# Kernel tuning notes

Measured on AMD Instinct MI355X. Metric: run time of the kernel, lower is better.

The kernel has to match this reference:

```python
import jax, jax.numpy as jnp
import numpy as np

TOP_K = 2  # num_active_experts


def setup_inputs() -> dict:
    key = jax.random.key(0)
    k1, k2, k3 = jax.random.split(key, 3)
    N, D, E = 16384, 1024, 8
    x = jax.random.normal(k1, (N, D), dtype=jnp.float32)
    router_w = jax.random.normal(k2, (E, D), dtype=jnp.float32) * (1.0 / np.sqrt(D))
    router_b = jnp.zeros((E,), dtype=jnp.float32)
    expert_w = jax.random.normal(k3, (E, D, D), dtype=jnp.float32) * (1.0 / np.sqrt(D))
    expert_b = jnp.zeros((E, D), dtype=jnp.float32)
    return {"x": x, "router_w": router_w, "router_b": router_b,
            "expert_w": expert_w, "expert_b": expert_b}


def reference(x, router_w, router_b, expert_w, expert_b):
    E = router_w.shape[0]
    # Router: softmax over experts, pick top-k, renormalize
    logits = x @ router_w.T + router_b                      # [N, E]
    probs = jax.nn.softmax(logits, axis=-1)                 # [N, E]
    top_p, top_i = jax.lax.top_k(probs, TOP_K)              # [N, K]
    top_p = top_p / jnp.sum(top_p, axis=-1, keepdims=True)  # renormalized gates
    # Dense combine weights: [N, E], zero for non-selected experts
    combine = jnp.sum(jax.nn.one_hot(top_i, E, dtype=x.dtype) * top_p[..., None], axis=1)
    # All-expert outputs, then weighted combine (vectorized dispatch/combine)
    y = jnp.einsum('nd,eod->neo', x, expert_w) + expert_b   # [N, E, O]
    out = jnp.einsum('neo,ne->no', y, combine)              # [N, O]
    return out
```

## Files before the change

kernel.cpp:

```cpp
#include <hip/hip_runtime.h>
#include <hip/hip_bf16.h>


constexpr int DIMS = 1024;
constexpr int NE   = 8;
constexpr int ROUTER_BLOCKS = 1024;
constexpr int WCONV_BLOCKS  = NE * DIMS * DIMS / (8 * 256);
constexpr int RT_PER_XCD = 33;

typedef __attribute__((ext_vector_type(8))) short short8;
typedef __attribute__((ext_vector_type(4))) short short4_t;
typedef __attribute__((ext_vector_type(4))) float f32x4;

typedef const __attribute__((address_space(1))) void* gp_t;
typedef __attribute__((address_space(3))) void* sp_t;

__device__ __forceinline__ float b2f(unsigned short u) {
  union { unsigned int i; float f; } x; x.i = ((unsigned)u) << 16; return x.f;
}
__device__ __forceinline__ short f2bs(float f) {
  __hip_bfloat16 h = __float2bfloat16(f);
  return *(short*)&h;
}

__global__ __launch_bounds__(256) void prep_kernel(
    const float* __restrict__ x, const float* __restrict__ rw,
    const float* __restrict__ rb, const float* __restrict__ ew,
    __hip_bfloat16* __restrict__ xb, __hip_bfloat16* __restrict__ wb,
    int* __restrict__ blk_cnt, int* __restrict__ tmp_meta,
    float* __restrict__ tmp_gate, int n_tok) {
  const int tid = threadIdx.x;

  if ((int)blockIdx.x >= ROUTER_BLOCKS) {
    unsigned g = (unsigned)(blockIdx.x - ROUTER_BLOCKS) * 256 + tid;
    int l  = g & 63;
    int kc = (g >> 6) & 31;
    int nb = (g >> 11) & 63;
    int e  = g >> 17;
    int row = nb * 16 + (l & 15);
    int kb  = kc * 32 + ((l >> 4) << 3);
    const float4* src = (const float4*)(ew + ((size_t)e << 20) + (size_t)row * DIMS + kb);
    float4 a = src[0], b = src[1];
    union { __hip_bfloat16 h[8]; float4 f; } u;
    u.h[0] = __float2bfloat16(a.x); u.h[1] = __float2bfloat16(a.y);
    u.h[2] = __float2bfloat16(a.z); u.h[3] = __float2bfloat16(a.w);
    u.h[4] = __float2bfloat16(b.x); u.h[5] = __float2bfloat16(b.y);
    u.h[6] = __float2bfloat16(b.z); u.h[7] = __float2bfloat16(b.w);
    ((float4*)wb)[g] = u.f;
    return;
  }

  __shared__ float s_rw[NE * DIMS];
  __shared__ int s_cnt[NE];
  __shared__ int s_e[32];
  __shared__ float s_g[32];
  __shared__ int s_pos[32];

  const float4* rw4g = (const float4*)rw;
  float4* s4 = (float4*)s_rw;
  for (int i = tid; i < NE * DIMS / 4; i += 256) s4[i] = rw4g[i];
  if (tid < NE) s_cnt[tid] = 0;
  __syncthreads();

  const float4* s_rw4 = (const float4*)s_rw;
  const int wave = tid >> 6, lane = tid & 63;
  for (int i = 0; i < 4; ++i) {
    int t = blockIdx.x * 16 + wave * 4 + i;
    const float4* xr = (const float4*)(x + (size_t)t * DIMS);
    short4_t* xw = (short4_t*)(xb + (size_t)t * DIMS);
    float a[NE];
#pragma unroll
    for (int e = 0; e < NE; ++e) a[e] = 0.f;
#pragma unroll
    for (int j = 0; j < 4; ++j) {
      float4 v = xr[lane + j * 64];
      short4_t p;
      p[0] = f2bs(v.x); p[1] = f2bs(v.y); p[2] = f2bs(v.z); p[3] = f2bs(v.w);
      xw[lane + j * 64] = p;
#pragma unroll
      for (int e = 0; e < NE; ++e) {
        float4 w = s_rw4[e * 256 + lane + j * 64];
        a[e] = fmaf(v.x, w.x, fmaf(v.y, w.y, fmaf(v.z, w.z, fmaf(v.w, w.w, a[e]))));
      }
    }
#pragma unroll
    for (int off = 32; off > 0; off >>= 1) {
#pragma unroll
      for (int e = 0; e < NE; ++e) a[e] += __shfl_xor(a[e], off, 64);
    }
    if (lane == 0) {
      float l[NE];
#pragma unroll
      for (int e = 0; e < NE; ++e) l[e] = a[e] + rb[e];
      int e0 = 0;
#pragma unroll
      for (int e = 1; e < NE; ++e) if (l[e] > l[e0]) e0 = e;
      int e1 = (e0 == 0) ? 1 : 0;
#pragma unroll
      for (int e = 0; e < NE; ++e) if (e != e0 && l[e] > l[e1]) e1 = e;
      float r = expf(l[e1] - l[e0]);
      float g0 = 1.f / (1.f + r);
      float g1 = 1.f - g0;
      int ai = (wave * 4 + i) * 2;
      int p0 = atomicAdd(&s_cnt[e0], 1);
      int p1 = atomicAdd(&s_cnt[e1], 1);
      s_e[ai] = e0; s_g[ai] = g0; s_pos[ai] = p0;
      s_e[ai + 1] = e1; s_g[ai + 1] = g1; s_pos[ai + 1] = p1;
    }
  }
  __syncthreads();
  if (tid < NE) blk_cnt[blockIdx.x * NE + tid] = s_cnt[tid];
  if (tid < 32) {
    int s = blockIdx.x * 32 + tid;
    tmp_meta[s] = s_e[tid] | (s_pos[tid] << 3);
    tmp_gate[s] = s_g[tid];
  }
}

__global__ __launch_bounds__(512) void scan_kernel(
    const int* __restrict__ blk_cnt, int* __restrict__ blk_base,
    int* __restrict__ counts) {
  const int e = threadIdx.x >> 6, lane = threadIdx.x & 63;
  int running = 0;
  for (int c = 0; c < ROUTER_BLOCKS / 64; ++c) {
    int v = blk_cnt[(c * 64 + lane) * NE + e];
    int incl = v;
#pragma unroll
    for (int off = 1; off < 64; off <<= 1) {
      int t = __shfl_up(incl, off, 64);
      if (lane >= off) incl += t;
    }
    blk_base[(c * 64 + lane) * NE + e] = running + incl - v;
    running += __shfl(incl, 63, 64);
  }
  if (lane == 0) counts[e] = running;
}

__global__ __launch_bounds__(256) void scatter_kernel(
    const int* __restrict__ tmp_meta, const float* __restrict__ tmp_gate,
    const int* __restrict__ blk_base, int* __restrict__ entries,
    float* __restrict__ gates, int n_tok) {
  int s = blockIdx.x * 256 + threadIdx.x;
  int meta = tmp_meta[s];
  int e = meta & 7, pos = meta >> 3;
  int p = blk_base[(s >> 5) * NE + e] + pos;
  entries[e * n_tok + p] = ((s >> 1) << 1) | (s & 1);
  gates[e * n_tok + p] = tmp_gate[s];
}

__global__ __launch_bounds__(256, 4) void moe_gemm(
    const __hip_bfloat16* __restrict__ xb, const __hip_bfloat16* __restrict__ wb,
    const float* __restrict__ eb, const int* __restrict__ counts,
    const int* __restrict__ entries, const float* __restrict__ gates,
    __hip_bfloat16* __restrict__ y, int n_tok) {
  const int xcd = blockIdx.x & 7;
  const int j = blockIdx.x >> 3;
  const int ct = j & 7;
  const int virt = xcd * RT_PER_XCD + (j >> 3);

  int e = -1, rt = 0, cnt = 0, acc_t = 0;
#pragma unroll
  for (int i = 0; i < NE; ++i) {
    int c = counts[i];
    int t = (c + 127) >> 7;
    if (e < 0 && virt < acc_t + t) { e = i; rt = virt - acc_t; cnt = c; }
    acc_t += t;
  }
  if (e < 0) return;

  __shared__ __hip_bfloat16 As[2][128 * 32];

  const int tid = threadIdx.x;
  const int lane = tid & 63, wave = tid >> 6;
  const int row0 = rt * 128;
  const int n0 = ct * 128;

  const int srow = tid >> 2;
  const int kcs = (tid & 3) ^ (srow & 3);
  const int kcol = kcs * 8;
  int gr0 = row0 + srow, gr1 = row0 + srow + 64;
  int ent0 = (gr0 < cnt) ? entries[e * n_tok + gr0] : 0;
  int ent1 = (gr1 < cnt) ? entries[e * n_tok + gr1] : 0;
  const __hip_bfloat16* ap0 = xb + (size_t)(ent0 >> 1) * DIMS + kcol;
  const __hip_bfloat16* ap1 = xb + (size_t)(ent1 >> 1) * DIMS + kcol;

  const int wm = (wave & 1) * 64, wn = (wave >> 1) * 64;
  const int fr = lane & 15, quad = lane >> 4;
  const int swo = (quad ^ (fr & 3)) * 8;

  const short8* wb8 = (const short8*)wb;
  const size_t bbase = (((size_t)e * 64 + ((n0 + wn) >> 4)) * 32) * 64 + lane;

  f32x4 acc[4][4] = {};

  __builtin_amdgcn_global_load_lds((gp_t)(ap0), (sp_t)(&As[0][tid * 8]), 16, 0, 0);
  __builtin_amdgcn_global_load_lds((gp_t)(ap1), (sp_t)(&As[0][(tid + 256) * 8]), 16, 0, 0);

#pragma unroll 1
  for (int ks = 0; ks < 32; ++ks) {
    const int cur = ks & 1;
    asm volatile("s_waitcnt vmcnt(0)" ::: "memory");
    __builtin_amdgcn_s_barrier();
    __builtin_amdgcn_sched_barrier(0);

    short8 bf[4];
#pragma unroll
    for (int nt = 0; nt < 4; ++nt)
      bf[nt] = wb8[bbase + (size_t)nt * 2048 + ks * 64];
    __builtin_amdgcn_sched_barrier(0);

    if (ks < 31) {
      __builtin_amdgcn_global_load_lds((gp_t)(ap0 + (ks + 1) * 32),
                                       (sp_t)(&As[cur ^ 1][tid * 8]), 16, 0, 0);
      __builtin_amdgcn_global_load_lds((gp_t)(ap1 + (ks + 1) * 32),
                                       (sp_t)(&As[cur ^ 1][(tid + 256) * 8]), 16, 0, 0);
    }

    short8 af[4];
#pragma unroll
    for (int mt = 0; mt < 4; ++mt)
      af[mt] = *(const short8*)&As[cur][(wm + mt * 16 + fr) * 32 + swo];
#pragma unroll
    for (int mt = 0; mt < 4; ++mt)
#pragma unroll
      for (int nt = 0; nt < 4; ++nt)
        acc[mt][nt] = __builtin_amdgcn_mfma_f32_16x16x32_bf16(af[mt], bf[nt], acc[mt][nt], 0, 0, 0);
  }

  float bias[4];
#pragma unroll
  for (int nt = 0; nt < 4; ++nt) bias[nt] = eb[e * DIMS + n0 + wn + nt * 16 + fr];
#pragma unroll
  for (int mt = 0; mt < 4; ++mt) {
#pragma unroll
    for (int r = 0; r < 4; ++r) {
      int m = wm + mt * 16 + quad * 4 + r;
      int gr = row0 + m;
      if (gr < cnt) {
        int ent = entries[e * n_tok + gr];
        float g = gates[e * n_tok + gr];
        __hip_bfloat16* yp = y + (size_t)ent * DIMS + n0 + wn + fr;
#pragma unroll
        for (int nt = 0; nt < 4; ++nt)
          yp[nt * 16] = __float2bfloat16(g * (acc[mt][nt][r] + bias[nt]));
      }
    }
  }
}

__global__ __launch_bounds__(256) void combine_kernel(const __hip_bfloat16* __restrict__ y,
                                                      float* __restrict__ out) {
  size_t idx = (size_t)blockIdx.x * 256 + threadIdx.x;
  size_t n = idx >> 7;
  int c = (int)(idx & 127) << 3;
  short8 v0 = *(const short8*)(y + (n * 2) * DIMS + c);
  short8 v1 = *(const short8*)(y + (n * 2 + 1) * DIMS + c);
  float4 o0, o1;
  o0.x = b2f((unsigned short)v0[0]) + b2f((unsigned short)v1[0]);
  o0.y = b2f((unsigned short)v0[1]) + b2f((unsigned short)v1[1]);
  o0.z = b2f((unsigned short)v0[2]) + b2f((unsigned short)v1[2]);
  o0.w = b2f((unsigned short)v0[3]) + b2f((unsigned short)v1[3]);
  o1.x = b2f((unsigned short)v0[4]) + b2f((unsigned short)v1[4]);
  o1.y = b2f((unsigned short)v0[5]) + b2f((unsigned short)v1[5]);
  o1.z = b2f((unsigned short)v0[6]) + b2f((unsigned short)v1[6]);
  o1.w = b2f((unsigned short)v0[7]) + b2f((unsigned short)v1[7]);
  float* op = out + n * DIMS + c;
  ((float4*)op)[0] = o0;
  ((float4*)op)[1] = o1;
}

extern "C" void kernel_launch(void* const* d_in, const int* in_sizes, int n_in,
                              void* d_out, int out_size, void* d_ws, size_t ws_size,
                              hipStream_t stream) {
  const float* x  = (const float*)d_in[0];
  const float* rw = (const float*)d_in[1];
  const float* rb = (const float*)d_in[2];
  const float* ew = (const float*)d_in[3];
  const float* eb = (const float*)d_in[4];
  float* out = (float*)d_out;
  const int n_tok = in_sizes[0] / DIMS;
  const int n_slot = 2 * n_tok;

  char* ws = (char*)d_ws;
  size_t off = 0;
  int* counts = (int*)ws;                      off += 256;
  int* blk_cnt = (int*)(ws + off);             off += (size_t)ROUTER_BLOCKS * NE * 4;
  int* blk_base = (int*)(ws + off);            off += (size_t)ROUTER_BLOCKS * NE * 4;
  int* tmp_meta = (int*)(ws + off);            off += (size_t)n_slot * 4;
  float* tmp_gate = (float*)(ws + off);        off += (size_t)n_slot * 4;
  __hip_bfloat16* xb = (__hip_bfloat16*)(ws + off); off += (size_t)n_tok * DIMS * 2;
  __hip_bfloat16* wb = (__hip_bfloat16*)(ws + off); off += (size_t)NE * DIMS * DIMS * 2;
  int*   entries = (int*)(ws + off);           off += (size_t)NE * n_tok * 4;
  float* gates   = (float*)(ws + off);         off += (size_t)NE * n_tok * 4;
  __hip_bfloat16* y = (__hip_bfloat16*)(ws + off); off += (size_t)n_slot * DIMS * 2;
  if (ws_size < off) return;

  prep_kernel<<<ROUTER_BLOCKS + WCONV_BLOCKS, 256, 0, stream>>>(
      x, rw, rb, ew, xb, wb, blk_cnt, tmp_meta, tmp_gate, n_tok);
  scan_kernel<<<1, 512, 0, stream>>>(blk_cnt, blk_base, counts);
  scatter_kernel<<<n_slot / 256, 256, 0, stream>>>(
      tmp_meta, tmp_gate, blk_base, entries, gates, n_tok);
  moe_gemm<<<8 * RT_PER_XCD * 8, 256, 0, stream>>>(
      xb, wb, eb, counts, entries, gates, y, n_tok);
  combine_kernel<<<(unsigned)((size_t)n_tok * DIMS / 8 / 256), 256, 0, stream>>>(y, out);
}
```

Measured before the change: 273.4 us.

## Stage expert weights through LDS and fold block scan into scatter

The weight conversion now writes bf16 weights in plain row-major order instead of a pre-swizzled MFMA fragment layout. The GEMM stages B tiles through double-buffered LDS with async global-to-LDS loads, the same way it handles A, replacing direct per-wave global fragment loads. The separate single-block scan kernel is removed: each scatter block recomputes its own per-expert prefix by summing earlier block counts, and block 0 writes the totals. This drops one launch and a serial scan at the cost of redundant prefix work and doubled LDS per GEMM block, which may reduce occupancy.

Result: slower. 279.6 us (+2.3%).

```diff
diff --git a/kernel.cpp b/kernel.cpp
--- a/kernel.cpp
+++ b/kernel.cpp
@@ -33,13 +33,7 @@
 
   if ((int)blockIdx.x >= ROUTER_BLOCKS) {
     unsigned g = (unsigned)(blockIdx.x - ROUTER_BLOCKS) * 256 + tid;
-    int l  = g & 63;
-    int kc = (g >> 6) & 31;
-    int nb = (g >> 11) & 63;
-    int e  = g >> 17;
-    int row = nb * 16 + (l & 15);
-    int kb  = kc * 32 + ((l >> 4) << 3);
-    const float4* src = (const float4*)(ew + ((size_t)e << 20) + (size_t)row * DIMS + kb);
+    const float4* src = (const float4*)(ew + (size_t)g * 8);
     float4 a = src[0], b = src[1];
     union { __hip_bfloat16 h[8]; float4 f; } u;
     u.h[0] = __float2bfloat16(a.x); u.h[1] = __float2bfloat16(a.y);
@@ -117,33 +111,48 @@
   }
 }
 
-__global__ __launch_bounds__(512) void scan_kernel(
-    const int* __restrict__ blk_cnt, int* __restrict__ blk_base,
-    int* __restrict__ counts) {
-  const int e = threadIdx.x >> 6, lane = threadIdx.x & 63;
-  int running = 0;
-  for (int c = 0; c < ROUTER_BLOCKS / 64; ++c) {
-    int v = blk_cnt[(c * 64 + lane) * NE + e];
-    int incl = v;
-#pragma unroll
-    for (int off = 1; off < 64; off <<= 1) {
-      int t = __shfl_up(incl, off, 64);
-      if (lane >= off) incl += t;
-    }
-    blk_base[(c * 64 + lane) * NE + e] = running + incl - v;
-    running += __shfl(incl, 63, 64);
-  }
-  if (lane == 0) counts[e] = running;
-}
-
 __global__ __launch_bounds__(256) void scatter_kernel(
-    const int* __restrict__ tmp_meta, const float* __restrict__ tmp_gate,
-    const int* __restrict__ blk_base, int* __restrict__ entries,
-    float* __restrict__ gates, int n_tok) {
-  int s = blockIdx.x * 256 + threadIdx.x;
+    const int* __restrict__ blk_cnt, const int* __restrict__ tmp_meta,
+    const float* __restrict__ tmp_gate, int* __restrict__ entries,
+    float* __restrict__ gates, int* __restrict__ counts, int n_tok) {
+  const int b = blockIdx.x;
+  const int t = threadIdx.x, lane = t & 63, wv = t >> 6;
+  __shared__ int s_base[8][NE];
+
+#pragma unroll
+  for (int ei = 0; ei < 2; ++ei) {
+    int e = wv * 2 + ei;
+    int M = b * 8;
+    int s = 0;
+    for (int idx = lane; idx < M; idx += 64) s += blk_cnt[idx * NE + e];
+#pragma unroll
+    for (int off = 32; off > 0; off >>= 1) s += __shfl_xor(s, off, 64);
+    if (lane == 0) {
+      int run = s;
+#pragma unroll
+      for (int i = 0; i < 8; ++i) {
+        s_base[i][e] = run;
+        run += blk_cnt[(b * 8 + i) * NE + e];
+      }
+    }
+  }
+  if (b == 0) {
+#pragma unroll
+    for (int ei = 0; ei < 2; ++ei) {
+      int e = wv * 2 + ei;
+      int s = 0;
+      for (int idx = lane; idx < ROUTER_BLOCKS; idx += 64) s += blk_cnt[idx * NE + e];
+#pragma unroll
+      for (int off = 32; off > 0; off >>= 1) s += __shfl_xor(s, off, 64);
+      if (lane == 0) counts[e] = s;
+    }
+  }
+  __syncthreads();
+
+  int s = b * 256 + t;
   int meta = tmp_meta[s];
   int e = meta & 7, pos = meta >> 3;
-  int p = blk_base[(s >> 5) * NE + e] + pos;
+  int p = s_base[(s >> 5) & 7][e] + pos;
   entries[e * n_tok + p] = ((s >> 1) << 1) | (s & 1);
   gates[e * n_tok + p] = tmp_gate[s];
 }
@@ -169,6 +178,7 @@
   if (e < 0) return;
 
   __shared__ __hip_bfloat16 As[2][128 * 32];
+  __shared__ __hip_bfloat16 Bs[2][128 * 32];
 
   const int tid = threadIdx.x;
   const int lane = tid & 63, wave = tid >> 6;
@@ -183,18 +193,19 @@
   int ent1 = (gr1 < cnt) ? entries[e * n_tok + gr1] : 0;
   const __hip_bfloat16* ap0 = xb + (size_t)(ent0 >> 1) * DIMS + kcol;
   const __hip_bfloat16* ap1 = xb + (size_t)(ent1 >> 1) * DIMS + kcol;
+  const __hip_bfloat16* bp0 = wb + ((size_t)e << 20) + (size_t)(n0 + srow) * DIMS + kcol;
+  const __hip_bfloat16* bp1 = bp0 + (size_t)64 * DIMS;
 
   const int wm = (wave & 1) * 64, wn = (wave >> 1) * 64;
   const int fr = lane & 15, quad = lane >> 4;
   const int swo = (quad ^ (fr & 3)) * 8;
 
-  const short8* wb8 = (const short8*)wb;
-  const size_t bbase = (((size_t)e * 64 + ((n0 + wn) >> 4)) * 32) * 64 + lane;
-
   f32x4 acc[4][4] = {};
 
   __builtin_amdgcn_global_load_lds((gp_t)(ap0), (sp_t)(&As[0][tid * 8]), 16, 0, 0);
   __builtin_amdgcn_global_load_lds((gp_t)(ap1), (sp_t)(&As[0][(tid + 256) * 8]), 16, 0, 0);
+  __builtin_amdgcn_global_load_lds((gp_t)(bp0), (sp_t)(&Bs[0][tid * 8]), 16, 0, 0);
+  __builtin_amdgcn_global_load_lds((gp_t)(bp1), (sp_t)(&Bs[0][(tid + 256) * 8]), 16, 0, 0);
 
 #pragma unroll 1
   for (int ks = 0; ks < 32; ++ks) {
@@ -203,23 +214,21 @@
     __builtin_amdgcn_s_barrier();
     __builtin_amdgcn_sched_barrier(0);
 
-    short8 bf[4];
-#pragma unroll
-    for (int nt = 0; nt < 4; ++nt)
-      bf[nt] = wb8[bbase + (size_t)nt * 2048 + ks * 64];
-    __builtin_amdgcn_sched_barrier(0);
-
     if (ks < 31) {
-      __builtin_amdgcn_global_load_lds((gp_t)(ap0 + (ks + 1) * 32),
-                                       (sp_t)(&As[cur ^ 1][tid * 8]), 16, 0, 0);
-      __builtin_amdgcn_global_load_lds((gp_t)(ap1 + (ks + 1) * 32),
-                                       (sp_t)(&As[cur ^ 1][(tid + 256) * 8]), 16, 0, 0);
-    }
-
-    short8 af[4];
+      const int ko = (ks + 1) * 32;
+      __builtin_amdgcn_global_load_lds((gp_t)(ap0 + ko), (sp_t)(&As[cur ^ 1][tid * 8]), 16, 0, 0);
+      __builtin_amdgcn_global_load_lds((gp_t)(ap1 + ko), (sp_t)(&As[cur ^ 1][(tid + 256) * 8]), 16, 0, 0);
+      __builtin_amdgcn_global_load_lds((gp_t)(bp0 + ko), (sp_t)(&Bs[cur ^ 1][tid * 8]), 16, 0, 0);
+      __builtin_amdgcn_global_load_lds((gp_t)(bp1 + ko), (sp_t)(&Bs[cur ^ 1][(tid + 256) * 8]), 16, 0, 0);
+    }
+
+    short8 af[4], bf[4];
 #pragma unroll
     for (int mt = 0; mt < 4; ++mt)
       af[mt] = *(const short8*)&As[cur][(wm + mt * 16 + fr) * 32 + swo];
+#pragma unroll
+    for (int nt = 0; nt < 4; ++nt)
+      bf[nt] = *(const short8*)&Bs[cur][(wn + nt * 16 + fr) * 32 + swo];
 #pragma unroll
     for (int mt = 0; mt < 4; ++mt)
 #pragma unroll
@@ -285,7 +294,6 @@
   size_t off = 0;
   int* counts = (int*)ws;                      off += 256;
   int* blk_cnt = (int*)(ws + off);             off += (size_t)ROUTER_BLOCKS * NE * 4;
-  int* blk_base = (int*)(ws + off);            off += (size_t)ROUTER_BLOCKS * NE * 4;
   int* tmp_meta = (int*)(ws + off);            off += (size_t)n_slot * 4;
   float* tmp_gate = (float*)(ws + off);        off += (size_t)n_slot * 4;
   __hip_bfloat16* xb = (__hip_bfloat16*)(ws + off); off += (size_t)n_tok * DIMS * 2;
@@ -297,9 +305,8 @@
 
   prep_kernel<<<ROUTER_BLOCKS + WCONV_BLOCKS, 256, 0, stream>>>(
       x, rw, rb, ew, xb, wb, blk_cnt, tmp_meta, tmp_gate, n_tok);
-  scan_kernel<<<1, 512, 0, stream>>>(blk_cnt, blk_base, counts);
   scatter_kernel<<<n_slot / 256, 256, 0, stream>>>(
-      tmp_meta, tmp_gate, blk_base, entries, gates, n_tok);
+      blk_cnt, tmp_meta, tmp_gate, entries, gates, counts, n_tok);
   moe_gemm<<<8 * RT_PER_XCD * 8, 256, 0, stream>>>(
       xb, wb, eb, counts, entries, gates, y, n_tok);
   combine_kernel<<<(unsigned)((size_t)n_tok * DIMS / 8 / 256), 256, 0, stream>>>(y, out);
```
